# Kernel tuning notes

Hardware: AMD Instinct MI355X
Metric: run time of the kernel (lower is better)

## Reference

```python
import jax, jax.numpy as jnp
import numpy as np

BN, DIM, HI, WI = 1, 192, 48, 48
E, N, P, HH = 384, 16, 64, 6      # d_inner, d_state, headdim, n_heads
HALF = N // 2                      # complex state pairs
K = 4                              # cross-scan directions
L = HI * WI


def _silu(v):
    return v * jax.nn.sigmoid(v)


def _rms(v, eps=1e-6):
    return v * jax.lax.rsqrt(jnp.mean(v * v, -1, keepdims=True) + eps)


def _mamba3(x, w_zx, w_bc, b_bc, w_dt, dt_bias, A_log, theta, D_skip, rms_w, w_mout):
    # x: (BK, L, E). Mamba3 core: no conv1d, rope-factored complex SSM,
    # trapezoidal discretization, qk-normed B/C, internal silu gate + gated RMSNorm.
    BK = x.shape[0]
    zx = x @ w_zx
    z, xi = zx[..., :E], zx[..., E:]
    bc = x @ w_bc + b_bc                                   # bc_bias
    Bm, Cm = _rms(bc[..., :N]), _rms(bc[..., N:])          # qk_norm
    dt = jax.nn.softplus(x @ w_dt + dt_bias)               # (BK,L,HH)
    r = jnp.exp(-dt * jnp.exp(A_log))                      # real decay per head
    ang = jnp.cumsum(dt, 1)[..., None] * theta             # (BK,L,HH,HALF) cumulative rope angle
    c, s = jnp.cos(ang), jnp.sin(ang)

    def rot(v):  # rotate state pairs by -ang (rope factoring of complex eigenvalues)
        vp = v.reshape(BK, -1, 1, HALF, 2)
        v0, v1 = vp[..., 0], vp[..., 1]
        return jnp.stack([v0 * c + v1 * s, -v0 * s + v1 * c], -1).reshape(BK, -1, HH, N)

    Bt, Ct = rot(Bm), rot(Cm)
    xh = xi.reshape(BK, -1, HH, P)
    u = jnp.einsum('blhn,blhp->blhnp', Bt, xh)             # (BK,L,HH,N,P)
    u_prev = jnp.pad(u[:, :-1], ((0, 0), (1, 0), (0, 0), (0, 0), (0, 0)))
    # trapezoidal rule: h_t = r_t h_{t-1} + dt_t/2 (B_t x_t + r_t B_{t-1} x_{t-1})
    inp = 0.5 * dt[..., None, None] * (u + r[..., None, None] * u_prev)

    def step(h, t):
        inp_t, r_t, C_t = t
        h = r_t[..., None, None] * h + inp_t
        return h, jnp.einsum('bhn,bhnp->bhp', C_t, h)

    h0 = jnp.zeros((BK, HH, N, P), x.dtype)
    _, ys = jax.lax.scan(step, h0, (inp.transpose(1, 0, 2, 3, 4), r.transpose(1, 0, 2), Ct.transpose(1, 0, 2, 3)))
    y = ys.transpose(1, 0, 2, 3) + D_skip[None, None, :, None] * xh
    y = y.reshape(BK, -1, E)
    g = _rms(y * _silu(z)) * rms_w                          # gated RMSNorm
    return g @ w_mout


def _forward(x, w_in, w_zx, w_bc, b_bc, w_dt, dt_bias, A_log, theta, D_skip, rms_w, w_mout, w_out, ln_g, ln_b, res_scale):
    Bn = x.shape[0]
    d0 = x.reshape(Bn, DIM, L)
    d1 = jnp.swapaxes(x, 2, 3).reshape(Bn, DIM, L)
    xs = jnp.stack([d0, d1, d0[..., ::-1], d1[..., ::-1]], 1)   # (B,4,C,L) cross-scan
    x_seq = xs.reshape(Bn * K, L, DIM)                          # matches torch .view memory reinterpret
    proj = x_seq @ w_in
    x_ssm, x_gate = proj[..., :E], proj[..., E:]
    x_ssm = _mamba3(_silu(x_ssm), w_zx, w_bc, b_bc, w_dt, dt_bias, A_log, theta, D_skip, rms_w, w_mout)
    x_out = x_ssm * _silu(x_gate)                               # (BK,L,E)
    yf = jnp.swapaxes(x_out, 1, 2).reshape(Bn, K, E, L)
    m1 = jnp.swapaxes(yf[:, 1].reshape(Bn, E, WI, HI), 2, 3).reshape(Bn, E, L)
    m3 = jnp.swapaxes(yf[:, 3, :, ::-1].reshape(Bn, E, WI, HI), 2, 3).reshape(Bn, E, L)
    merged = yf[:, 0] + m1 + yf[:, 2, :, ::-1] + m3             # cross-merge
    merged = merged.reshape(Bn, E, HI, WI)
    out = jnp.einsum('behw,ed->bdhw', merged, w_out)            # 1x1 conv out_proj
    out = jnp.moveaxis(out, 1, -1)
    mu = jnp.mean(out, -1, keepdims=True)
    var = jnp.mean((out - mu) ** 2, -1, keepdims=True)
    out = (out - mu) * jax.lax.rsqrt(var + 1e-5) * ln_g + ln_b  # LayerNorm
    out = jnp.moveaxis(out, -1, 1)
    return x + res_scale[0] * out


def setup_inputs() -> dict:
    key = jax.random.key(0)
    ks = jax.random.split(key, 16)
    f = jax.random.normal
    return {
        'x': f(ks[0], (BN, DIM, HI, WI), jnp.float32),
        'w_in': f(ks[1], (DIM, 2 * E)) * 0.05,
        'w_zx': f(ks[2], (E, 2 * E)) * 0.05,
        'w_bc': f(ks[3], (E, 2 * N)) * 0.05,
        'b_bc': f(ks[4], (2 * N,)) * 0.05,
        'w_dt': f(ks[5], (E, HH)) * 0.05,
        'dt_bias': f(ks[6], (HH,)) * 0.5,
        'A_log': f(ks[7], (HH,)) * 0.5,
        'theta': f(ks[8], (HH, HALF)),
        'D_skip': f(ks[9], (HH,)) * 0.5,
        'rms_w': jnp.ones((E,)),
        'w_mout': f(ks[10], (E, E)) * 0.05,
        'w_out': f(ks[11], (E, DIM)) * 0.05,
        'ln_g': jnp.ones((DIM,)),
        'ln_b': jnp.zeros((DIM,)),
        'res_scale': jnp.full((1,), 0.5),
    }


def reference(x, w_in, w_zx, w_bc, b_bc, w_dt, dt_bias, A_log, theta, D_skip, rms_w, w_mout, w_out, ln_g, ln_b, res_scale):
    return _forward(x, w_in, w_zx, w_bc, b_bc, w_dt, dt_bias, A_log, theta, D_skip, rms_w, w_mout, w_out, ln_g, ln_b, res_scale)
```

## Files before the change

### kernel.cpp

```cpp
#include <hip/hip_runtime.h>
#include <hip/hip_bf16.h>
#include <math.h>

#define BN   1
#define DIMC 192
#define HI   48
#define WI   48
#define LL   2304
#define EE   384
#define NN   16
#define PP   64
#define HHH  6
#define HALF 8
#define KK   4
#define BK_SEQ (BN*KK)
#define NBH  (BK_SEQ*HHH)
#define CLEN 24
#define NCHUNK 96
#define ZLD  896

typedef __attribute__((ext_vector_type(8))) short bf16x8;
typedef __attribute__((ext_vector_type(4))) float f32x4;

static __device__ __forceinline__ float siluf(float v) {
    return v / (1.f + expf(-v));
}
static __device__ __forceinline__ unsigned short f2bf(float f) {
    unsigned int u = __float_as_uint(f);
    u = (u + 0x7FFFu + ((u >> 16) & 1u)) >> 16;
    return (unsigned short)u;
}

#define NP0 (KK*LL*DIMC)
#define NP1 (768*DIMC)
#define NP2 (ZLD*EE)
#define NP2b 896
#define NP3 (EE*EE)
#define NP4 (256*EE)
#define NPTOT (NP0+NP1+NP2+NP2b+NP3+NP4)

__global__ __launch_bounds__(256) void k_prep_all(const float* __restrict__ x,
                                                  const float* __restrict__ w_in,
                                                  const float* __restrict__ w_zx,
                                                  const float* __restrict__ w_bc,
                                                  const float* __restrict__ w_dt,
                                                  const float* __restrict__ b_bc,
                                                  const float* __restrict__ dt_bias,
                                                  const float* __restrict__ w_mout,
                                                  const float* __restrict__ w_out,
                                                  unsigned short* __restrict__ xseq,
                                                  unsigned short* __restrict__ winT,
                                                  unsigned short* __restrict__ wcatT,
                                                  float* __restrict__ biascat,
                                                  unsigned short* __restrict__ wmoT,
                                                  unsigned short* __restrict__ woT) {
    int idx = blockIdx.x * 256 + threadIdx.x;
    if (idx < NP0) {
        int d = idx % DIMC;
        int l = (idx / DIMC) % LL;
        int k = idx / (DIMC * LL);
        int dim = l / 12;
        int pos = (l % 12) * DIMC + d;
        int src;
        if (k == 0)      src = pos;
        else if (k == 1) src = (pos % 48) * 48 + pos / 48;
        else if (k == 2) src = 2303 - pos;
        else { int p2 = 2303 - pos; src = (p2 % 48) * 48 + p2 / 48; }
        xseq[idx] = f2bf(x[dim * LL + src]);
        return;
    }
    idx -= NP0;
    if (idx < NP1) {
        int r = idx % DIMC;
        int c = idx / DIMC;
        winT[idx] = f2bf(w_in[(size_t)r * 768 + c]);
        return;
    }
    idx -= NP1;
    if (idx < NP2) {
        int n = idx / EE, k = idx % EE;
        float v = 0.f;
        if (n < 768)      v = w_zx[(size_t)k * 768 + n];
        else if (n < 800) v = w_bc[(size_t)k * 32 + (n - 768)];
        else if (n < 806) v = w_dt[(size_t)k * 6 + (n - 800)];
        wcatT[idx] = f2bf(v);
        return;
    }
    idx -= NP2;
    if (idx < NP2b) {
        float v = 0.f;
        if (idx >= 768 && idx < 800) v = b_bc[idx - 768];
        else if (idx >= 800 && idx < 806) v = dt_bias[idx - 800];
        biascat[idx] = v;
        return;
    }
    idx -= NP2b;
    if (idx < NP3) {
        int r = idx % EE;
        int c = idx / EE;
        wmoT[idx] = f2bf(w_mout[(size_t)r * EE + c]);
        return;
    }
    idx -= NP3;
    if (idx < NP4) {
        int d = idx / EE, e = idx % EE;
        woT[idx] = (d < DIMC) ? f2bf(w_out[(size_t)e * DIMC + d]) : (unsigned short)0;
    }
}

template <int EPI>
__global__ __launch_bounds__(256) void gemm_bf16(const unsigned short* __restrict__ A,
                                                 const unsigned short* __restrict__ BT,
                                                 const float* __restrict__ bias,
                                                 float* __restrict__ C,
                                                 unsigned short* __restrict__ X,
                                                 int K, int lda, int ldbt, int ldc) {
    __shared__ __align__(16) unsigned short As[2][64][40];
    __shared__ __align__(16) unsigned short Bs[2][128][40];
    int bm = blockIdx.y * 64, bn = blockIdx.x * 128;
    int tid = threadIdx.x;
    int lane = tid & 63, wave = tid >> 6;
    int wn = wave * 32;
    f32x4 acc[4][2];
#pragma unroll
    for (int f = 0; f < 4; f++)
#pragma unroll
        for (int g = 0; g < 2; g++) acc[f][g] = (f32x4){0.f, 0.f, 0.f, 0.f};

    int fr = lane & 15;
    int kl = (lane >> 4) * 8;

    int sr = tid >> 2;
    int sq = (tid & 3) * 8;
    const unsigned short* aptr  = A + (size_t)(bm + sr) * lda + sq;
    const unsigned short* bptr0 = BT + (size_t)(bn + sr) * ldbt + sq;
    const unsigned short* bptr1 = BT + (size_t)(bn + sr + 64) * ldbt + sq;

    uint4 pa  = *(const uint4*)aptr;
    uint4 pb0 = *(const uint4*)bptr0;
    uint4 pb1 = *(const uint4*)bptr1;
    *(uint4*)&As[0][sr][sq]      = pa;
    *(uint4*)&Bs[0][sr][sq]      = pb0;
    *(uint4*)&Bs[0][sr + 64][sq] = pb1;
    if (K > 32) {
        pa  = *(const uint4*)(aptr + 32);
        pb0 = *(const uint4*)(bptr0 + 32);
        pb1 = *(const uint4*)(bptr1 + 32);
    }
    __syncthreads();

    for (int k0 = 0; k0 < K; k0 += 32) {
        int cur = (k0 >> 5) & 1;
        bf16x8 af[4], bg[2];
#pragma unroll
        for (int f = 0; f < 4; f++) af[f] = *(const bf16x8*)&As[cur][f * 16 + fr][kl];
#pragma unroll
        for (int g = 0; g < 2; g++) bg[g] = *(const bf16x8*)&Bs[cur][wn + g * 16 + fr][kl];
        if (k0 + 32 < K) {
            *(uint4*)&As[cur ^ 1][sr][sq]      = pa;
            *(uint4*)&Bs[cur ^ 1][sr][sq]      = pb0;
            *(uint4*)&Bs[cur ^ 1][sr + 64][sq] = pb1;
        }
        if (k0 + 64 < K) {
            pa  = *(const uint4*)(aptr + k0 + 64);
            pb0 = *(const uint4*)(bptr0 + k0 + 64);
            pb1 = *(const uint4*)(bptr1 + k0 + 64);
        }
        __syncthreads();
#pragma unroll
        for (int f = 0; f < 4; f++)
#pragma unroll
            for (int g = 0; g < 2; g++)
                acc[f][g] = __builtin_amdgcn_mfma_f32_16x16x32_bf16(af[f], bg[g], acc[f][g], 0, 0, 0);
    }
    int cc = lane & 15, crb = (lane >> 4) * 4;
    if (EPI == 0) {
#pragma unroll
        for (int f = 0; f < 4; f++)
#pragma unroll
            for (int g = 0; g < 2; g++) {
                int col = bn + wn + g * 16 + cc;
                float bv = bias ? bias[col] : 0.f;
#pragma unroll
                for (int i = 0; i < 4; i++)
                    C[(size_t)(bm + f * 16 + crb + i) * ldc + col] = acc[f][g][i] + bv;
            }
    } else {
#pragma unroll
        for (int f = 0; f < 4; f++)
#pragma unroll
            for (int g = 0; g < 2; g++) {
                int col = bn + wn + g * 16 + cc;
                if (col < 384) {
#pragma unroll
                    for (int i = 0; i < 4; i++)
                        X[(size_t)(bm + f * 16 + crb + i) * 384 + col] =
                            f2bf(siluf(acc[f][g][i]));
                } else {
#pragma unroll
                    for (int i = 0; i < 4; i++)
                        C[(size_t)(bm + f * 16 + crb + i) * 384 + col - 384] =
                            siluf(acc[f][g][i]);
                }
            }
    }
}

__global__ __launch_bounds__(256) void k_dtcum(const float* __restrict__ zxb,
                                               const float* __restrict__ A_log,
                                               float* __restrict__ dtv,
                                               float* __restrict__ rrv,
                                               float* __restrict__ cum) {
    int bh = blockIdx.x;
    int tid = threadIdx.x;
    int b = bh / HHH, h = bh % HHH;
    float aexp = expf(A_log[h]);
    const int PER = 9;
    int base = tid * PER;
    float p[PER];
    float s = 0.f;
#pragma unroll
    for (int j = 0; j < PER; j++) {
        int l = base + j;
        float xv = zxb[((size_t)b * LL + l) * ZLD + 800 + h];
        float sp = fmaxf(xv, 0.f) + log1pf(expf(-fabsf(xv)));
        dtv[(size_t)bh * LL + l] = sp;
        rrv[(size_t)bh * LL + l] = expf(-sp * aexp);
        s += sp; p[j] = s;
    }
    __shared__ float sh[256];
    sh[tid] = s;
    __syncthreads();
    for (int off = 1; off < 256; off <<= 1) {
        float t = (tid >= off) ? sh[tid - off] : 0.f;
        __syncthreads();
        sh[tid] += t;
        __syncthreads();
    }
    float excl = sh[tid] - s;
#pragma unroll
    for (int j = 0; j < PER; j++) cum[(size_t)bh * LL + base + j] = excl + p[j];
}

__global__ __launch_bounds__(256) void k_rot(const float* __restrict__ zxb,
                                             const float* __restrict__ cum,
                                             const float* __restrict__ theta,
                                             float* __restrict__ btct) {
    int idx = blockIdx.x * 256 + threadIdx.x;
    if (idx >= NBH * LL) return;
    int bh = idx / LL, l = idx % LL;
    int b = bh / HHH, h = bh % HHH;
    const float* bcrow = zxb + ((size_t)b * LL + l) * ZLD + 768;
    float Bm[16], Cm[16];
    float sb = 0.f, sc = 0.f;
#pragma unroll
    for (int j = 0; j < 16; j++) {
        Bm[j] = bcrow[j];      sb += Bm[j] * Bm[j];
        Cm[j] = bcrow[16 + j]; sc += Cm[j] * Cm[j];
    }
    float rb = rsqrtf(sb * (1.f / 16.f) + 1e-6f);
    float rc = rsqrtf(sc * (1.f / 16.f) + 1e-6f);
    float cd = cum[(size_t)bh * LL + l];
    float* out = btct + ((size_t)bh * LL + l) * 32;
#pragma unroll
    for (int j = 0; j < 8; j++) {
        float ang = cd * theta[h * 8 + j];
        float cc = cosf(ang), ss = sinf(ang);
        float b0 = Bm[2 * j] * rb, b1 = Bm[2 * j + 1] * rb;
        out[2 * j]     = b0 * cc + b1 * ss;
        out[2 * j + 1] = -b0 * ss + b1 * cc;
        float c0 = Cm[2 * j] * rc, c1 = Cm[2 * j + 1] * rc;
        out[16 + 2 * j]     = c0 * cc + c1 * ss;
        out[16 + 2 * j + 1] = -c0 * ss + c1 * cc;
    }
}

template <int MODE>
__global__ __launch_bounds__(64) void k_scan_phase(const float* __restrict__ btct,
                                                   const float* __restrict__ rrv,
                                                   const float* __restrict__ dtv,
                                                   const float* __restrict__ zxb,
                                                   const float* __restrict__ h0,
                                                   float* __restrict__ Hc,
                                                   float* __restrict__ Rc,
                                                   float* __restrict__ yD,
                                                   const float* __restrict__ Dsk) {
    int chunk = blockIdx.x;
    int bh = blockIdx.y;
    int lane = threadIdx.x;
    int b = bh / HHH, h = bh % HHH;
    int t0 = chunk * CLEN;

    __shared__ float sbt[(CLEN + 1) * 32];
    __shared__ float srd[2 * CLEN];

    const float* bt_row = btct + (size_t)bh * LL * 32;
    for (int i = lane; i < (CLEN + 1) * 8; i += 64) {
        int t = t0 - 1 + (i >> 3);
        float4 v = make_float4(0.f, 0.f, 0.f, 0.f);
        if (t >= 0)
            v = ((const float4*)(bt_row + (size_t)t * 32))[i & 7];
        ((float4*)sbt)[i] = v;
    }
    if (lane < CLEN) {
        srd[lane] = rrv[(size_t)bh * LL + t0 + lane];
        srd[CLEN + lane] = 0.5f * dtv[(size_t)bh * LL + t0 + lane];
    }

    const float* xcol = zxb + (size_t)b * LL * ZLD + EE + h * PP + lane;
    float xr[CLEN];
#pragma unroll
    for (int j = 0; j < CLEN; j++) xr[j] = xcol[(size_t)(t0 + j) * ZLD];
    float xprev = (t0 > 0) ? xcol[(size_t)(t0 - 1) * ZLD] : 0.f;

    float hreg[16];
    if (MODE == 0) {
#pragma unroll
        for (int n = 0; n < 16; n++) hreg[n] = 0.f;
    } else {
        const float* hp = h0 + ((size_t)(chunk * NBH + bh) * 16) * PP + lane;
#pragma unroll
        for (int n = 0; n < 16; n++) hreg[n] = hp[n * PP];
    }
    float dsk = (MODE == 1) ? Dsk[h] : 0.f;
    __syncthreads();

    float Btp[16];
#pragma unroll
    for (int n = 0; n < 16; n++) Btp[n] = sbt[n];
    float Rprod = 1.f;

#pragma unroll
    for (int j = 0; j < CLEN; j++) {
        float r = srd[j];
        float dhalf = srd[CLEN + j];
        float xcur = xr[j];
        const float* bb = sbt + (j + 1) * 32;
        float a = dhalf * xcur;
        float ap = dhalf * r * xprev;
        float y = 0.f;
#pragma unroll
        for (int n = 0; n < 16; n++) {
            float Btn = bb[n];
            hreg[n] = r * hreg[n] + a * Btn + ap * Btp[n];
            Btp[n] = Btn;
            if (MODE) y += bb[16 + n] * hreg[n];
        }
        xprev = xcur;
        if (MODE) {
            yD[((size_t)b * LL + t0 + j) * EE + h * PP + lane] = y + dsk * xcur;
        } else {
            Rprod *= r;
        }
    }
    if (MODE == 0) {
        float* Hp = Hc + ((size_t)(chunk * NBH + bh) * 16) * PP + lane;
#pragma unroll
        for (int n = 0; n < 16; n++) Hp[n * PP] = hreg[n];
        if (lane == 0) Rc[chunk * NBH + bh] = Rprod;
    }
}

__global__ __launch_bounds__(64) void k_scan_combine(const float* __restrict__ Hc,
                                                     const float* __restrict__ Rc,
                                                     float* __restrict__ h0) {
    int bh = blockIdx.x;
    int lane = threadIdx.x;
    float s[16];
#pragma unroll
    for (int n = 0; n < 16; n++) s[n] = 0.f;
    float* out0 = h0 + ((size_t)(0 * NBH + bh) * 16) * PP + lane;
#pragma unroll
    for (int n = 0; n < 16; n++) out0[n * PP] = 0.f;
    for (int c = 0; c < NCHUNK - 1; ++c) {
        float R = Rc[c * NBH + bh];
        const float* Hp = Hc + ((size_t)(c * NBH + bh) * 16) * PP + lane;
        float* op = h0 + ((size_t)((c + 1) * NBH + bh) * 16) * PP + lane;
#pragma unroll
        for (int n = 0; n < 16; n++) {
            s[n] = R * s[n] + Hp[n * PP];
            op[n * PP] = s[n];
        }
    }
}

__global__ __launch_bounds__(128) void k_gmul(const float* __restrict__ yD,
                                              const float* __restrict__ zxb,
                                              const float* __restrict__ rms_w,
                                              unsigned short* __restrict__ g) {
    int row = blockIdx.x;
    int tid = threadIdx.x;
    int lane = tid & 63, wid = tid >> 6;
    float v[3];
    float ss = 0.f;
#pragma unroll
    for (int j = 0; j < 3; j++) {
        int e = tid * 3 + j;
        float y = yD[(size_t)row * EE + e];
        float z = zxb[(size_t)row * ZLD + e];
        v[j] = y * siluf(z);
        ss += v[j] * v[j];
    }
#pragma unroll
    for (int off = 1; off < 64; off <<= 1) ss += __shfl_xor(ss, off);
    __shared__ float red[2];
    if (lane == 0) red[wid] = ss;
    __syncthreads();
    float total = red[0] + red[1];
    float scale = rsqrtf(total * (1.f / (float)EE) + 1e-6f);
#pragma unroll
    for (int j = 0; j < 3; j++) {
        int e = tid * 3 + j;
        g[(size_t)row * EE + e] = f2bf(v[j] * scale * rms_w[e]);
    }
}

__global__ __launch_bounds__(256) void k_merge(const float* __restrict__ mres,
                                               const float* __restrict__ gsil,
                                               unsigned short* __restrict__ mrg) {
    int idx = blockIdx.x * 256 + threadIdx.x;
    if (idx >= LL * EE) return;
    int e = idx % EE, l = idx / EE;
    int l1 = (l % 48) * 48 + l / 48;
    int rows[4];
    rows[0] = 0 * LL + l;
    rows[1] = 1 * LL + l1;
    rows[2] = 2 * LL + (2303 - l);
    rows[3] = 3 * LL + (2303 - l1);
    float acc = 0.f;
#pragma unroll
    for (int k = 0; k < 4; k++) {
        float m = mres[(size_t)rows[k] * EE + e];
        float gz = gsil[(size_t)rows[k] * EE + e];
        acc += m * gz;
    }
    mrg[idx] = f2bf(acc);
}

__global__ __launch_bounds__(64) void k_ln(const float* __restrict__ outT,
                                           const float* __restrict__ x,
                                           const float* __restrict__ ln_g,
                                           const float* __restrict__ ln_b,
                                           const float* __restrict__ res_scale,
                                           float* __restrict__ outF) {
    int l = blockIdx.x;
    int lane = threadIdx.x;
    float v[3];
    float s = 0.f;
#pragma unroll
    for (int j = 0; j < 3; j++) {
        int d = lane * 3 + j;
        v[j] = outT[(size_t)l * 256 + d];
        s += v[j];
    }
#pragma unroll
    for (int off = 1; off < 64; off <<= 1) s += __shfl_xor(s, off);
    float mu = s * (1.f / (float)DIMC);
    float sq = 0.f;
#pragma unroll
    for (int j = 0; j < 3; j++) { float dlt = v[j] - mu; sq += dlt * dlt; }
#pragma unroll
    for (int off = 1; off < 64; off <<= 1) sq += __shfl_xor(sq, off);
    float rstd = rsqrtf(sq * (1.f / (float)DIMC) + 1e-5f);
    float rs = res_scale[0];
#pragma unroll
    for (int j = 0; j < 3; j++) {
        int d = lane * 3 + j;
        outF[(size_t)d * LL + l] =
            x[(size_t)d * LL + l] + rs * ((v[j] - mu) * rstd * ln_g[d] + ln_b[d]);
    }
}

extern "C" void kernel_launch(void* const* d_in, const int* in_sizes, int n_in,
                              void* d_out, int out_size, void* d_ws, size_t ws_size,
                              hipStream_t stream) {
    const float* x        = (const float*)d_in[0];
    const float* w_in     = (const float*)d_in[1];
    const float* w_zx     = (const float*)d_in[2];
    const float* w_bc     = (const float*)d_in[3];
    const float* b_bc     = (const float*)d_in[4];
    const float* w_dt     = (const float*)d_in[5];
    const float* dt_bias  = (const float*)d_in[6];
    const float* A_log    = (const float*)d_in[7];
    const float* theta    = (const float*)d_in[8];
    const float* D_skip   = (const float*)d_in[9];
    const float* rms_w    = (const float*)d_in[10];
    const float* w_mout   = (const float*)d_in[11];
    const float* w_out    = (const float*)d_in[12];
    const float* ln_g     = (const float*)d_in[13];
    const float* ln_b     = (const float*)d_in[14];
    const float* res_scale= (const float*)d_in[15];
    float* outF = (float*)d_out;
    float* ws = (float*)d_ws;

    size_t o = 0;
    auto alloc = [&](size_t n) { size_t r = o; o += (n + 127) & ~(size_t)127; return r; };
    size_t xseqb_o = alloc((size_t)9216 * DIMC / 2);
    size_t winT_o  = alloc((size_t)768 * DIMC / 2);
    size_t wcatT_o = alloc((size_t)ZLD * EE / 2);
    size_t wmoT_o  = alloc((size_t)384 * 384 / 2);
    size_t woT_o   = alloc((size_t)256 * EE / 2);
    size_t bcat_o  = alloc(ZLD);
    size_t xact_o  = alloc((size_t)9216 * EE / 2);
    size_t gsil_o  = alloc((size_t)9216 * EE);
    size_t zxb_o   = alloc((size_t)9216 * ZLD);
    size_t btct_o  = alloc((size_t)NBH * LL * 32);
    size_t dtv_o   = alloc((size_t)NBH * LL);
    size_t rrv_o   = alloc((size_t)NBH * LL);
    size_t cum_o   = alloc((size_t)NBH * LL);
    size_t Hc_o    = alloc((size_t)NCHUNK * NBH * 16 * PP);
    size_t Rc_o    = alloc((size_t)NCHUNK * NBH);
    size_t h0_o    = alloc((size_t)NCHUNK * NBH * 16 * PP);
    size_t yD_o    = alloc((size_t)9216 * EE);
    size_t mrg_o   = alloc((size_t)LL * EE / 2);
    size_t outT_o  = alloc((size_t)LL * 256);

    unsigned short* xseqb = (unsigned short*)(ws + xseqb_o);
    unsigned short* winT  = (unsigned short*)(ws + winT_o);
    unsigned short* wcatT = (unsigned short*)(ws + wcatT_o);
    unsigned short* wmoT  = (unsigned short*)(ws + wmoT_o);
    unsigned short* woT   = (unsigned short*)(ws + woT_o);
    float* bcat = ws + bcat_o;
    unsigned short* xact = (unsigned short*)(ws + xact_o);
    float* gsil = ws + gsil_o;
    float* zxb  = ws + zxb_o;
    float* btct = ws + btct_o;
    float* dtv  = ws + dtv_o;
    float* rrv  = ws + rrv_o;
    float* cum  = ws + cum_o;
    float* Hc   = ws + Hc_o;
    float* Rc   = ws + Rc_o;
    float* h0   = ws + h0_o;
    float* yD   = ws + yD_o;
    unsigned short* mrg = (unsigned short*)(ws + mrg_o);
    float* outT = ws + outT_o;
    float* mres = zxb;
    unsigned short* g_bf = xact;

    k_prep_all<<<(NPTOT + 255) / 256, 256, 0, stream>>>(
        x, w_in, w_zx, w_bc, w_dt, b_bc, dt_bias, w_mout, w_out,
        xseqb, winT, wcatT, bcat, wmoT, woT);
    gemm_bf16<1><<<dim3(768 / 128, 9216 / 64), 256, 0, stream>>>(
        xseqb, winT, nullptr, gsil, xact, DIMC, DIMC, DIMC, 0);
    gemm_bf16<0><<<dim3(ZLD / 128, 9216 / 64), 256, 0, stream>>>(
        xact, wcatT, bcat, zxb, nullptr, EE, EE, EE, ZLD);
    k_dtcum<<<NBH, 256, 0, stream>>>(zxb, A_log, dtv, rrv, cum);
    k_rot<<<(NBH * LL + 255) / 256, 256, 0, stream>>>(zxb, cum, theta, btct);
    k_scan_phase<0><<<dim3(NCHUNK, NBH), 64, 0, stream>>>(btct, rrv, dtv, zxb, h0, Hc, Rc, yD, D_skip);
    k_scan_combine<<<NBH, 64, 0, stream>>>(Hc, Rc, h0);
    k_scan_phase<1><<<dim3(NCHUNK, NBH), 64, 0, stream>>>(btct, rrv, dtv, zxb, h0, Hc, Rc, yD, D_skip);
    k_gmul<<<9216, 128, 0, stream>>>(yD, zxb, rms_w, g_bf);
    gemm_bf16<0><<<dim3(384 / 128, 9216 / 64), 256, 0, stream>>>(
        g_bf, wmoT, nullptr, mres, nullptr, 384, 384, 384, 384);
    k_merge<<<(LL * EE + 255) / 256, 256, 0, stream>>>(mres, gsil, mrg);
    gemm_bf16<0><<<dim3(256 / 128, LL / 64), 256, 0, stream>>>(
        mrg, woT, nullptr, outT, nullptr, EE, EE, EE, 256);
    k_ln<<<LL, 64, 0, stream>>>(outT, x, ln_g, ln_b, res_scale, outF);
    (void)in_sizes; (void)n_in; (void)out_size; (void)ws_size;
}
```

Before: 163.6 us.

## Store intermediate activations in bf16 and split zx/bc/dt GEMM outputs

Result: faster. 158.3 us, median of 2 (-3.2%).

```diff
diff --git a/kernel.cpp b/kernel.cpp
--- a/kernel.cpp
+++ b/kernel.cpp
@@ -29,6 +29,9 @@
     unsigned int u = __float_as_uint(f);
     u = (u + 0x7FFFu + ((u >> 16) & 1u)) >> 16;
     return (unsigned short)u;
+}
+static __device__ __forceinline__ float bf2f(unsigned short u) {
+    return __uint_as_float((unsigned int)u << 16);
 }
 
 #define NP0 (KK*LL*DIMC)
@@ -114,6 +117,7 @@
                                                  const float* __restrict__ bias,
                                                  float* __restrict__ C,
                                                  unsigned short* __restrict__ X,
+                                                 unsigned short* __restrict__ Y,
                                                  int K, int lda, int ldbt, int ldc) {
     __shared__ __align__(16) unsigned short As[2][64][40];
     __shared__ __align__(16) unsigned short Bs[2][128][40];
@@ -174,39 +178,51 @@
                 acc[f][g] = __builtin_amdgcn_mfma_f32_16x16x32_bf16(af[f], bg[g], acc[f][g], 0, 0, 0);
     }
     int cc = lane & 15, crb = (lane >> 4) * 4;
-    if (EPI == 0) {
-#pragma unroll
-        for (int f = 0; f < 4; f++)
-#pragma unroll
-            for (int g = 0; g < 2; g++) {
-                int col = bn + wn + g * 16 + cc;
+#pragma unroll
+    for (int f = 0; f < 4; f++)
+#pragma unroll
+        for (int g = 0; g < 2; g++) {
+            int col = bn + wn + g * 16 + cc;
+            int rowb = bm + f * 16 + crb;
+            if (EPI == 0) {
                 float bv = bias ? bias[col] : 0.f;
 #pragma unroll
                 for (int i = 0; i < 4; i++)
-                    C[(size_t)(bm + f * 16 + crb + i) * ldc + col] = acc[f][g][i] + bv;
+                    C[(size_t)(rowb + i) * ldc + col] = acc[f][g][i] + bv;
+            } else if (EPI == 1) {
+                if (col < 384) {
+#pragma unroll
+                    for (int i = 0; i < 4; i++)
+                        X[(size_t)(rowb + i) * 384 + col] = f2bf(siluf(acc[f][g][i]));
+                } else {
+#pragma unroll
+                    for (int i = 0; i < 4; i++)
+                        Y[(size_t)(rowb + i) * 384 + col - 384] = f2bf(siluf(acc[f][g][i]));
+                }
+            } else if (EPI == 2) {
+                if (col < 384) {
+#pragma unroll
+                    for (int i = 0; i < 4; i++)
+                        X[(size_t)(rowb + i) * 384 + col] = f2bf(siluf(acc[f][g][i]));
+                } else if (col < 768) {
+#pragma unroll
+                    for (int i = 0; i < 4; i++)
+                        Y[(size_t)(rowb + i) * 384 + col - 384] = f2bf(acc[f][g][i]);
+                } else {
+                    float bv = bias[col];
+#pragma unroll
+                    for (int i = 0; i < 4; i++)
+                        C[(size_t)(rowb + i) * 128 + col - 768] = acc[f][g][i] + bv;
+                }
+            } else {
+#pragma unroll
+                for (int i = 0; i < 4; i++)
+                    X[(size_t)(rowb + i) * ldc + col] = f2bf(acc[f][g][i]);
             }
-    } else {
-#pragma unroll
-        for (int f = 0; f < 4; f++)
-#pragma unroll
-            for (int g = 0; g < 2; g++) {
-                int col = bn + wn + g * 16 + cc;
-                if (col < 384) {
-#pragma unroll
-                    for (int i = 0; i < 4; i++)
-                        X[(size_t)(bm + f * 16 + crb + i) * 384 + col] =
-                            f2bf(siluf(acc[f][g][i]));
-                } else {
-#pragma unroll
-                    for (int i = 0; i < 4; i++)
-                        C[(size_t)(bm + f * 16 + crb + i) * 384 + col - 384] =
-                            siluf(acc[f][g][i]);
-                }
-            }
-    }
-}
-
-__global__ __launch_bounds__(256) void k_dtcum(const float* __restrict__ zxb,
+        }
+}
+
+__global__ __launch_bounds__(256) void k_dtcum(const float* __restrict__ bcdt,
                                                const float* __restrict__ A_log,
                                                float* __restrict__ dtv,
                                                float* __restrict__ rrv,
@@ -222,7 +238,7 @@
 #pragma unroll
     for (int j = 0; j < PER; j++) {
         int l = base + j;
-        float xv = zxb[((size_t)b * LL + l) * ZLD + 800 + h];
+        float xv = bcdt[((size_t)b * LL + l) * 128 + 32 + h];
         float sp = fmaxf(xv, 0.f) + log1pf(expf(-fabsf(xv)));
         dtv[(size_t)bh * LL + l] = sp;
         rrv[(size_t)bh * LL + l] = expf(-sp * aexp);
@@ -242,7 +258,7 @@
     for (int j = 0; j < PER; j++) cum[(size_t)bh * LL + base + j] = excl + p[j];
 }
 
-__global__ __launch_bounds__(256) void k_rot(const float* __restrict__ zxb,
+__global__ __launch_bounds__(256) void k_rot(const float* __restrict__ bcdt,
                                              const float* __restrict__ cum,
                                              const float* __restrict__ theta,
                                              float* __restrict__ btct) {
@@ -250,7 +266,7 @@
     if (idx >= NBH * LL) return;
     int bh = idx / LL, l = idx % LL;
     int b = bh / HHH, h = bh % HHH;
-    const float* bcrow = zxb + ((size_t)b * LL + l) * ZLD + 768;
+    const float* bcrow = bcdt + ((size_t)b * LL + l) * 128;
     float Bm[16], Cm[16];
     float sb = 0.f, sc = 0.f;
 #pragma unroll
@@ -279,11 +295,11 @@
 __global__ __launch_bounds__(64) void k_scan_phase(const float* __restrict__ btct,
                                                    const float* __restrict__ rrv,
                                                    const float* __restrict__ dtv,
-                                                   const float* __restrict__ zxb,
+                                                   const unsigned short* __restrict__ xhb,
                                                    const float* __restrict__ h0,
                                                    float* __restrict__ Hc,
                                                    float* __restrict__ Rc,
-                                                   float* __restrict__ yD,
+                                                   unsigned short* __restrict__ yDb,
                                                    const float* __restrict__ Dsk) {
     int chunk = blockIdx.x;
     int bh = blockIdx.y;
@@ -307,11 +323,11 @@
         srd[CLEN + lane] = 0.5f * dtv[(size_t)bh * LL + t0 + lane];
     }
 
-    const float* xcol = zxb + (size_t)b * LL * ZLD + EE + h * PP + lane;
+    const unsigned short* xcol = xhb + (size_t)b * LL * EE + h * PP + lane;
     float xr[CLEN];
 #pragma unroll
-    for (int j = 0; j < CLEN; j++) xr[j] = xcol[(size_t)(t0 + j) * ZLD];
-    float xprev = (t0 > 0) ? xcol[(size_t)(t0 - 1) * ZLD] : 0.f;
+    for (int j = 0; j < CLEN; j++) xr[j] = bf2f(xcol[(size_t)(t0 + j) * EE]);
+    float xprev = (t0 > 0) ? bf2f(xcol[(size_t)(t0 - 1) * EE]) : 0.f;
 
     float hreg[16];
     if (MODE == 0) {
@@ -348,7 +364,7 @@
         }
         xprev = xcur;
         if (MODE) {
-            yD[((size_t)b * LL + t0 + j) * EE + h * PP + lane] = y + dsk * xcur;
+            yDb[((size_t)b * LL + t0 + j) * EE + h * PP + lane] = f2bf(y + dsk * xcur);
         } else {
             Rprod *= r;
         }
@@ -384,8 +400,8 @@
     }
 }
 
-__global__ __launch_bounds__(128) void k_gmul(const float* __restrict__ yD,
-                                              const float* __restrict__ zxb,
+__global__ __launch_bounds__(128) void k_gmul(const unsigned short* __restrict__ yDb,
+                                              const unsigned short* __restrict__ zsil,
                                               const float* __restrict__ rms_w,
                                               unsigned short* __restrict__ g) {
     int row = blockIdx.x;
@@ -396,9 +412,9 @@
 #pragma unroll
     for (int j = 0; j < 3; j++) {
         int e = tid * 3 + j;
-        float y = yD[(size_t)row * EE + e];
-        float z = zxb[(size_t)row * ZLD + e];
-        v[j] = y * siluf(z);
+        float y = bf2f(yDb[(size_t)row * EE + e]);
+        float zs = bf2f(zsil[(size_t)row * EE + e]);
+        v[j] = y * zs;
         ss += v[j] * v[j];
     }
 #pragma unroll
@@ -415,8 +431,8 @@
     }
 }
 
-__global__ __launch_bounds__(256) void k_merge(const float* __restrict__ mres,
-                                               const float* __restrict__ gsil,
+__global__ __launch_bounds__(256) void k_merge(const unsigned short* __restrict__ mresb,
+                                               const unsigned short* __restrict__ gsil,
                                                unsigned short* __restrict__ mrg) {
     int idx = blockIdx.x * 256 + threadIdx.x;
     if (idx >= LL * EE) return;
@@ -430,8 +446,8 @@
     float acc = 0.f;
 #pragma unroll
     for (int k = 0; k < 4; k++) {
-        float m = mres[(size_t)rows[k] * EE + e];
-        float gz = gsil[(size_t)rows[k] * EE + e];
+        float m = bf2f(mresb[(size_t)rows[k] * EE + e]);
+        float gz = bf2f(gsil[(size_t)rows[k] * EE + e]);
         acc += m * gz;
     }
     mrg[idx] = f2bf(acc);
@@ -502,16 +518,18 @@
     size_t woT_o   = alloc((size_t)256 * EE / 2);
     size_t bcat_o  = alloc(ZLD);
     size_t xact_o  = alloc((size_t)9216 * EE / 2);
-    size_t gsil_o  = alloc((size_t)9216 * EE);
-    size_t zxb_o   = alloc((size_t)9216 * ZLD);
-    size_t btct_o  = alloc((size_t)NBH * LL * 32);
+    size_t gsil_o  = alloc((size_t)9216 * EE / 2);
+    size_t zsil_o  = alloc((size_t)9216 * EE / 2);
+    size_t xhb_o   = alloc((size_t)9216 * EE / 2);
+    size_t bcdt_o  = alloc((size_t)9216 * 128);
     size_t dtv_o   = alloc((size_t)NBH * LL);
     size_t rrv_o   = alloc((size_t)NBH * LL);
     size_t cum_o   = alloc((size_t)NBH * LL);
+    size_t btct_o  = alloc((size_t)NBH * LL * 32);
     size_t Hc_o    = alloc((size_t)NCHUNK * NBH * 16 * PP);
     size_t Rc_o    = alloc((size_t)NCHUNK * NBH);
     size_t h0_o    = alloc((size_t)NCHUNK * NBH * 16 * PP);
-    size_t yD_o    = alloc((size_t)9216 * EE);
+    size_t yDb_o   = alloc((size_t)9216 * EE / 2);
     size_t mrg_o   = alloc((size_t)LL * EE / 2);
     size_t outT_o  = alloc((size_t)LL * 256);
 
@@ -522,39 +540,41 @@
     unsigned short* woT   = (unsigned short*)(ws + woT_o);
     float* bcat = ws + bcat_o;
     unsigned short* xact = (unsigned short*)(ws + xact_o);
-    float* gsil = ws + gsil_o;
-    float* zxb  = ws + zxb_o;
-    float* btct = ws + btct_o;
+    unsigned short* gsil = (unsigned short*)(ws + gsil_o);
+    unsigned short* zsil = (unsigned short*)(ws + zsil_o);
+    unsigned short* xhb  = (unsigned short*)(ws + xhb_o);
+    float* bcdt = ws + bcdt_o;
     float* dtv  = ws + dtv_o;
     float* rrv  = ws + rrv_o;
     float* cum  = ws + cum_o;
+    float* btct = ws + btct_o;
     float* Hc   = ws + Hc_o;
     float* Rc   = ws + Rc_o;
     float* h0   = ws + h0_o;
-    float* yD   = ws + yD_o;
+    unsigned short* yDb = (unsigned short*)(ws + yDb_o);
     unsigned short* mrg = (unsigned short*)(ws + mrg_o);
     float* outT = ws + outT_o;
-    float* mres = zxb;
-    unsigned short* g_bf = xact;
+    unsigned short* g_bf  = xact;
+    unsigned short* mresb = zsil;
 
     k_prep_all<<<(NPTOT + 255) / 256, 256, 0, stream>>>(
         x, w_in, w_zx, w_bc, w_dt, b_bc, dt_bias, w_mout, w_out,
         xseqb, winT, wcatT, bcat, wmoT, woT);
     gemm_bf16<1><<<dim3(768 / 128, 9216 / 64), 256, 0, stream>>>(
-        xseqb, winT, nullptr, gsil, xact, DIMC, DIMC, DIMC, 0);
-    gemm_bf16<0><<<dim3(ZLD / 128, 9216 / 64), 256, 0, stream>>>(
-        xact, wcatT, bcat, zxb, nullptr, EE, EE, EE, ZLD);
-    k_dtcum<<<NBH, 256, 0, stream>>>(zxb, A_log, dtv, rrv, cum);
-    k_rot<<<(NBH * LL + 255) / 256, 256, 0, stream>>>(zxb, cum, theta, btct);
-    k_scan_phase<0><<<dim3(NCHUNK, NBH), 64, 0, stream>>>(btct, rrv, dtv, zxb, h0, Hc, Rc, yD, D_skip);
+        xseqb, winT, nullptr, nullptr, xact, gsil, DIMC, DIMC, DIMC, 0);
+    gemm_bf16<2><<<dim3(ZLD / 128, 9216 / 64), 256, 0, stream>>>(
+        xact, wcatT, bcat, bcdt, zsil, xhb, EE, EE, EE, 0);
+    k_dtcum<<<NBH, 256, 0, stream>>>(bcdt, A_log, dtv, rrv, cum);
+    k_rot<<<(NBH * LL + 255) / 256, 256, 0, stream>>>(bcdt, cum, theta, btct);
+    k_scan_phase<0><<<dim3(NCHUNK, NBH), 64, 0, stream>>>(btct, rrv, dtv, xhb, h0, Hc, Rc, yDb, D_skip);
     k_scan_combine<<<NBH, 64, 0, stream>>>(Hc, Rc, h0);
-    k_scan_phase<1><<<dim3(NCHUNK, NBH), 64, 0, stream>>>(btct, rrv, dtv, zxb, h0, Hc, Rc, yD, D_skip);
-    k_gmul<<<9216, 128, 0, stream>>>(yD, zxb, rms_w, g_bf);
-    gemm_bf16<0><<<dim3(384 / 128, 9216 / 64), 256, 0, stream>>>(
-        g_bf, wmoT, nullptr, mres, nullptr, 384, 384, 384, 384);
-    k_merge<<<(LL * EE + 255) / 256, 256, 0, stream>>>(mres, gsil, mrg);
+    k_scan_phase<1><<<dim3(NCHUNK, NBH), 64, 0, stream>>>(btct, rrv, dtv, xhb, h0, Hc, Rc, yDb, D_skip);
+    k_gmul<<<9216, 128, 0, stream>>>(yDb, zsil, rms_w, g_bf);
+    gemm_bf16<3><<<dim3(384 / 128, 9216 / 64), 256, 0, stream>>>(
+        g_bf, wmoT, nullptr, nullptr, mresb, nullptr, 384, 384, 384, 384);
+    k_merge<<<(LL * EE + 255) / 256, 256, 0, stream>>>(mresb, gsil, mrg);
     gemm_bf16<0><<<dim3(256 / 128, LL / 64), 256, 0, stream>>>(
-        mrg, woT, nullptr, outT, nullptr, EE, EE, EE, 256);
+        mrg, woT, nullptr, outT, nullptr, nullptr, EE, EE, EE, 256);
     k_ln<<<LL, 64, 0, stream>>>(outT, x, ln_g, ln_b, res_scale, outF);
     (void)in_sizes; (void)n_in; (void)out_size; (void)ws_size;
 }
```
